# Optimization experiments

Hardware: AMD Instinct MI355X
Metric: run time of the kernel (lower is better)

The kernel has to match this reference:

```python
import jax, jax.numpy as jnp
import numpy as np

H = 256  # LSTM hidden units per layer

def _cell(xt, h, c, W, U, b):
    # Keras LSTMCell: gate order i, f, g(cell), o; sigmoid recurrent activation, tanh activation
    z = xt @ W + h @ U + b  # (B, 4H)
    i, f, g, o = jnp.split(z, 4, axis=-1)
    c_new = jax.nn.sigmoid(f) * c + jax.nn.sigmoid(i) * jnp.tanh(g)
    h_new = jax.nn.sigmoid(o) * jnp.tanh(c_new)
    return h_new, c_new

def _stacked_lstm(x, W1, U1, b1, W2, U2, b2):
    # x: (B, T, F). Returns concat of FINAL CELL STATES of both layers: (B, 2H)
    # (original code takes outputs[i+1][1], i.e. the c state of each LSTMCell)
    B = x.shape[0]
    def step(carry, xt):
        h1, c1, h2, c2 = carry
        h1, c1 = _cell(xt, h1, c1, W1, U1, b1)
        h2, c2 = _cell(h1, h2, c2, W2, U2, b2)
        return (h1, c1, h2, c2), None
    z0 = jnp.zeros((B, H), x.dtype)
    (h1, c1, h2, c2), _ = jax.lax.scan(step, (z0, z0, z0, z0), jnp.swapaxes(x, 0, 1))
    return jnp.concatenate([c1, c2], axis=-1)

def _glorot(key, shape):
    lim = np.sqrt(6.0 / (shape[0] + shape[1]))
    return jax.random.uniform(key, shape, jnp.float32, -lim, lim)

def _lstm_bias():
    # Keras unit_forget_bias=True: forget-gate bias initialized to 1
    return jnp.zeros((4 * H,), jnp.float32).at[H:2 * H].set(1.0)

def setup_inputs():
    key = jax.random.key(0)
    ks = jax.random.split(key, 16)
    B, T, F, ZD = 16384, 20, 80, 32
    inp = {
        "x": jax.random.normal(ks[0], (B, T, F), jnp.float32),
        "eps1": jax.random.normal(ks[1], (B, ZD), jnp.float32),
        "eps2": jax.random.normal(ks[2], (B, ZD), jnp.float32),
        # z2 stacked LSTM (input F)
        "z2_W1": _glorot(ks[3], (F, 4 * H)), "z2_U1": _glorot(ks[4], (H, 4 * H)), "z2_b1": _lstm_bias(),
        "z2_W2": _glorot(ks[5], (H, 4 * H)), "z2_U2": _glorot(ks[6], (H, 4 * H)), "z2_b2": _lstm_bias(),
        # z1 stacked LSTM (input F + z2_dim)
        "z1_W1": _glorot(ks[7], (F + ZD, 4 * H)), "z1_U1": _glorot(ks[8], (H, 4 * H)), "z1_b1": _lstm_bias(),
        "z1_W2": _glorot(ks[9], (H, 4 * H)), "z1_U2": _glorot(ks[10], (H, 4 * H)), "z1_b2": _lstm_bias(),
        # dense heads (input 2H -> ZD), linear (mu_nl=logvar_nl=None)
        "mu2_W": _glorot(ks[11], (2 * H, ZD)), "mu2_b": jnp.zeros((ZD,), jnp.float32),
        "lv2_W": _glorot(ks[12], (2 * H, ZD)), "lv2_b": jnp.zeros((ZD,), jnp.float32),
        "mu1_W": _glorot(ks[13], (2 * H, ZD)), "mu1_b": jnp.zeros((ZD,), jnp.float32),
        "lv1_W": _glorot(ks[14], (2 * H, ZD)), "lv1_b": jnp.zeros((ZD,), jnp.float32),
    }
    return inp

def reference(x, eps1, eps2,
              z2_W1, z2_U1, z2_b1, z2_W2, z2_U2, z2_b2,
              z1_W1, z1_U1, z1_b1, z1_W2, z1_U2, z1_b2,
              mu2_W, mu2_b, lv2_W, lv2_b, mu1_W, mu1_b, lv1_W, lv1_b):
    B, T, _ = x.shape
    # z2 branch
    z2_pre = _stacked_lstm(x, z2_W1, z2_U1, z2_b1, z2_W2, z2_U2, z2_b2)  # (B, 2H)
    z2_mu = z2_pre @ mu2_W + mu2_b
    z2_logvar = z2_pre @ lv2_W + lv2_b
    z2_sample = eps2 * jnp.exp(0.5 * z2_logvar) + z2_mu  # reparameterize
    # z1 branch: tile z2_sample over time, concat with x
    z2_tiled = jnp.broadcast_to(z2_sample[:, None, :], (B, T, z2_sample.shape[-1]))
    x_z2 = jnp.concatenate([x, z2_tiled], axis=-1)  # (B, T, F+ZD)
    z1_pre = _stacked_lstm(x_z2, z1_W1, z1_U1, z1_b1, z1_W2, z1_U2, z1_b2)
    z1_mu = z1_pre @ mu1_W + mu1_b
    z1_logvar = z1_pre @ lv1_W + lv1_b
    z1_sample = eps1 * jnp.exp(0.5 * z1_logvar) + z1_mu
    return (z1_mu, z1_logvar, z1_sample, z2_mu, z2_logvar, z2_sample)
```

## Files before the change

### kernel.cpp

```cpp
#include <hip/hip_runtime.h>
#include <hip/hip_bf16.h>

#define B_SZ 16384
#define T_SZ 20

typedef __attribute__((ext_vector_type(8))) __bf16 bf16x8;
typedef __attribute__((ext_vector_type(4))) float f32x4;

__device__ __forceinline__ float sigm(float x){ return 1.f/(1.f+__expf(-x)); }
__device__ __forceinline__ float tanh_(float x){ return 1.f-2.f/(__expf(2.f*x)+1.f); }

#define OFF_L1Z2 0
#define OFF_L2Z2 360448
#define OFF_L1Z1 884736
#define OFF_L2Z1 1277952
#define OFF_HZ2  1802240
#define OFF_HZ1  1835008
#define WP_TOT   1867776

__global__ void prep_w(const float* __restrict__ W0, const float* __restrict__ U0,
                       const float* __restrict__ W1, const float* __restrict__ U1,
                       const float* __restrict__ W2, const float* __restrict__ U2,
                       const float* __restrict__ W3, const float* __restrict__ U3,
                       const float* __restrict__ muW2, const float* __restrict__ lvW2,
                       const float* __restrict__ muW1, const float* __restrict__ lvW1,
                       __bf16* __restrict__ wp)
{
    int idx = blockIdx.x * 256 + threadIdx.x;
    if (idx >= WP_TOT) return;
    if (idx < OFF_HZ2) {
        const float *W, *U;
        int Fx, Kx, KT, local;
        if (idx < OFF_L2Z2)      { W = W0; U = U0; Fx = 80;  Kx = 96;  KT = 11; local = idx; }
        else if (idx < OFF_L1Z1) { W = W1; U = U1; Fx = 256; Kx = 256; KT = 16; local = idx - OFF_L2Z2; }
        else if (idx < OFF_L2Z1) { W = W2; U = U2; Fx = 112; Kx = 128; KT = 12; local = idx - OFF_L1Z1; }
        else                     { W = W3; U = U3; Fx = 256; Kx = 256; KT = 16; local = idx - OFF_L2Z1; }
        int jj = local & 7, lane = (local >> 3) & 63, nt16 = (local >> 9) & 15, rest = local >> 13;
        int kt = rest % KT, wgn = rest / KT;
        int gate = nt16 & 3, hh = nt16 >> 2;
        int n = gate * 256 + wgn * 64 + hh * 16 + (lane & 15);
        int k = kt * 32 + ((lane >> 4) << 3) + jj;
        float v = (k < Fx) ? W[k * 1024 + n] : (k < Kx ? 0.f : U[(k - Kx) * 1024 + n]);
        wp[idx] = (__bf16)v;
    } else {
        int base = (idx < OFF_HZ1) ? OFF_HZ2 : OFF_HZ1;
        const float* mw = (idx < OFF_HZ1) ? muW2 : muW1;
        const float* lw = (idx < OFF_HZ1) ? lvW2 : lvW1;
        int local = idx - base;
        int jj = local & 7, lane = (local >> 3) & 63, nt = (local >> 9) & 3, kt = local >> 11;
        int k = kt * 32 + ((lane >> 4) << 3) + jj;
        int c16 = lane & 15;
        float v = (nt < 2) ? mw[k * 32 + nt * 16 + c16] : lw[k * 32 + (nt - 2) * 16 + c16];
        wp[idx] = (__bf16)v;
    }
}

__global__ void xconv(const float* __restrict__ x, __bf16* __restrict__ xb)
{
    int idx = blockIdx.x * 256 + threadIdx.x;
    int c8 = idx & 15, row = idx >> 4;
    bf16x8 r;
    if (c8 < 10) {
        const float4* p = reinterpret_cast<const float4*>(x + (size_t)row * 80 + c8 * 8);
        float4 u0 = p[0], u1 = p[1];
        r[0]=(__bf16)u0.x; r[1]=(__bf16)u0.y; r[2]=(__bf16)u0.z; r[3]=(__bf16)u0.w;
        r[4]=(__bf16)u1.x; r[5]=(__bf16)u1.y; r[6]=(__bf16)u1.z; r[7]=(__bf16)u1.w;
    } else {
#pragma unroll
        for (int i = 0; i < 8; ++i) r[i] = (__bf16)0.f;
    }
    *reinterpret_cast<bf16x8*>(xb + (size_t)row * 128 + c8 * 8) = r;
}

__global__ void bcast_z2(const __bf16* __restrict__ z2sb, __bf16* __restrict__ xb)
{
    int idx = blockIdx.x * 256 + threadIdx.x;
    int g = idx & 3, b = idx >> 2;
    bf16x8 v = *reinterpret_cast<const bf16x8*>(z2sb + (size_t)b * 32 + g * 8);
#pragma unroll
    for (int t = 0; t < T_SZ; ++t)
        *reinterpret_cast<bf16x8*>(xb + ((size_t)b * T_SZ + t) * 128 + 80 + g * 8) = v;
}

__device__ __forceinline__ void stage16(const __bf16* g, __bf16* l)
{
    __builtin_amdgcn_global_load_lds(
        (const __attribute__((address_space(1))) unsigned*)g,
        (__attribute__((address_space(3))) unsigned*)l, 16, 0, 0);
}

template <int KT, int KTP, int XKT, int TWOH, int FIRST>
__global__ void __launch_bounds__(512, 2)
step_gemm(const __bf16* __restrict__ xb, int t,
          const __bf16* __restrict__ hA, const __bf16* __restrict__ hB,
          const __bf16* __restrict__ wpm, const float* __restrict__ bias,
          float* __restrict__ cbuf, __bf16* __restrict__ hout)
{
    __shared__ __align__(16) __bf16 As[3][8192];

    const int tid = threadIdx.x;
    const int w = tid >> 6, lane = tid & 63;
    const int r16 = lane & 15, kq = lane >> 4;
    const int wr = w >> 2, wc = w & 3;
    const int mid = blockIdx.x & 63, wgn = blockIdx.x >> 6;
    const int rb = mid * 256;
    const __bf16* wpB = wpm + (size_t)wgn * KTP * 8192;
    const __bf16* pBW = wpB + wc * 2048 + lane * 8;

    const int srow0 = rb + w * 32 + (lane >> 2);
    const int ksub  = (lane & 3) * 8;
    const __bf16* pA0 = hA + (size_t)srow0 * 256 + ksub;
    const __bf16* pA1 = hA + (size_t)(srow0 + 16) * 256 + ksub;
    const __bf16* px0 = (XKT > 0) ? xb + ((size_t)srow0 * T_SZ + t) * 128 + ksub : pA0;
    const __bf16* px1 = (XKT > 0) ? xb + ((size_t)(srow0 + 16) * T_SZ + t) * 128 + ksub : pA1;
    const __bf16* pH0 = TWOH ? hB + (size_t)srow0 * 256 + ksub : pA0;
    const __bf16* pH1 = TWOH ? hB + (size_t)(srow0 + 16) * 256 + ksub : pA1;

    f32x4 acc[4][8];
#pragma unroll
    for (int g = 0; g < 4; ++g)
#pragma unroll
        for (int m = 0; m < 8; ++m) acc[g][m] = f32x4{0.f, 0.f, 0.f, 0.f};

    bf16x8 bR[3][4];

#define ASRC(K, P0, PA, PH_) \
    ((K) < XKT ? (P0) + (K) * 32 \
               : ((!TWOH || ((K) - XKT) < 8) ? (PA) + ((K) - XKT) * 32 \
                                             : (PH_) + ((K) - XKT - 8) * 32))
#define STG_A(K) { stage16(ASRC(K, px0, pA0, pH0), &As[(K) % 3][w * 1024]); \
                   stage16(ASRC(K, px1, pA1, pH1), &As[(K) % 3][w * 1024 + 512]); }
#define LDB(K) { _Pragma("unroll") for (int nt = 0; nt < 4; ++nt) \
                   bR[(K) % 3][nt] = *reinterpret_cast<const bf16x8*>(pBW + (size_t)(K) * 8192 + nt * 512); }
#define CMP(K) { const __bf16* ab_ = &As[(K) % 3][(wr * 128 + r16) * 32 + kq * 8]; \
    bf16x8 a_[8]; \
    _Pragma("unroll") for (int m = 0; m < 8; ++m) \
        a_[m] = *reinterpret_cast<const bf16x8*>(ab_ + m * 512); \
    _Pragma("unroll") for (int m = 0; m < 8; ++m) \
        _Pragma("unroll") for (int g = 0; g < 4; ++g) \
            acc[g][m] = __builtin_amdgcn_mfma_f32_16x16x32_bf16(a_[m], bR[(K) % 3][g], acc[g][m], 0, 0, 0); }
#define PH(K) if constexpr ((K) < KT) { \
    __builtin_amdgcn_sched_barrier(0); \
    if constexpr ((K) + 1 < KT) STG_A((K) + 1); \
    if constexpr ((K) + 2 < KT) LDB((K) + 2); \
    { constexpr int c_ = 2 * (((K) + 1 < KT) ? 1 : 0) + 4 * (((K) + 2 < KT) ? 1 : 0); \
      asm volatile("s_waitcnt vmcnt(%0)" :: "n"(c_) : "memory"); } \
    __builtin_amdgcn_s_barrier(); \
    __builtin_amdgcn_sched_barrier(0); \
    CMP(K); }

    STG_A(0); LDB(0);
    if constexpr (KT > 1) LDB(1);

    PH(0)  PH(1)  PH(2)  PH(3)  PH(4)  PH(5)  PH(6)  PH(7)
    PH(8)  PH(9)  PH(10) PH(11) PH(12) PH(13) PH(14) PH(15)

#undef ASRC
#undef STG_A
#undef LDB
#undef CMP
#undef PH

    const int hcol = wgn * 64 + wc * 16 + r16;
    float bg[4];
#pragma unroll
    for (int g = 0; g < 4; ++g) bg[g] = bias[g * 256 + hcol];

#pragma unroll
    for (int m = 0; m < 8; ++m) {
        f32x4 zi = acc[0][m], zf = acc[1][m], zg = acc[2][m], zo = acc[3][m];
#pragma unroll
        for (int q = 0; q < 4; ++q) {
            int row = rb + wr * 128 + m * 16 + kq * 4 + q;
            size_t off = (size_t)row * 256 + hcol;
            float cn;
            if (FIRST) {
                cn = sigm(zi[q] + bg[0]) * tanh_(zg[q] + bg[2]);
            } else {
                float co = cbuf[off];
                cn = sigm(zf[q] + bg[1]) * co + sigm(zi[q] + bg[0]) * tanh_(zg[q] + bg[2]);
            }
            cbuf[off] = cn;
            hout[off] = (__bf16)(sigm(zo[q] + bg[3]) * tanh_(cn));
        }
    }
}

__global__ void __launch_bounds__(128, 4)
head_mfma(const float* __restrict__ c1, const float* __restrict__ c2,
          const __bf16* __restrict__ hp, const float* __restrict__ mub,
          const float* __restrict__ lvb, const float* __restrict__ eps,
          float* __restrict__ omu, float* __restrict__ olv, float* __restrict__ osm,
          __bf16* __restrict__ osb)
{
    const int tid = threadIdx.x;
    const int w = tid >> 6, lane = tid & 63;
    const int r16 = lane & 15, kq = lane >> 4;
    const int rb = blockIdx.x * 64 + w * 32;

    f32x4 acc[4][2];
#pragma unroll
    for (int nt = 0; nt < 4; ++nt)
#pragma unroll
        for (int m = 0; m < 2; ++m) acc[nt][m] = f32x4{0.f, 0.f, 0.f, 0.f};

#pragma unroll
    for (int kt = 0; kt < 16; ++kt) {
        const float* cs = (kt < 8) ? c1 : c2;
        int k = (kt & 7) * 32 + kq * 8;
        bf16x8 a[2];
#pragma unroll
        for (int m = 0; m < 2; ++m) {
            const float* pr = cs + (size_t)(rb + m * 16 + r16) * 256 + k;
            float4 u0 = reinterpret_cast<const float4*>(pr)[0];
            float4 u1 = reinterpret_cast<const float4*>(pr)[1];
            a[m][0]=(__bf16)u0.x; a[m][1]=(__bf16)u0.y; a[m][2]=(__bf16)u0.z; a[m][3]=(__bf16)u0.w;
            a[m][4]=(__bf16)u1.x; a[m][5]=(__bf16)u1.y; a[m][6]=(__bf16)u1.z; a[m][7]=(__bf16)u1.w;
        }
        const __bf16* hb = hp + kt * 2048 + lane * 8;
#pragma unroll
        for (int nt = 0; nt < 4; ++nt) {
            bf16x8 bv = *reinterpret_cast<const bf16x8*>(hb + nt * 512);
            acc[nt][0] = __builtin_amdgcn_mfma_f32_16x16x32_bf16(a[0], bv, acc[nt][0], 0, 0, 0);
            acc[nt][1] = __builtin_amdgcn_mfma_f32_16x16x32_bf16(a[1], bv, acc[nt][1], 0, 0, 0);
        }
    }

#pragma unroll
    for (int m = 0; m < 2; ++m)
#pragma unroll
        for (int q = 0; q < 4; ++q) {
            int row = rb + m * 16 + kq * 4 + q;
#pragma unroll
            for (int z = 0; z < 2; ++z) {
                int zc = z * 16 + r16;
                float mu = acc[z][m][q] + mub[zc];
                float lv = acc[z + 2][m][q] + lvb[zc];
                int idx = row * 32 + zc;
                omu[idx] = mu;
                olv[idx] = lv;
                float s = fmaf(eps[idx], expf(0.5f * lv), mu);
                osm[idx] = s;
                if (osb) osb[idx] = (__bf16)s;
            }
        }
}

extern "C" void kernel_launch(void* const* d_in, const int* in_sizes, int n_in,
                              void* d_out, int out_size, void* d_ws, size_t ws_size,
                              hipStream_t stream)
{
    const float* x    = (const float*)d_in[0];
    const float* eps1 = (const float*)d_in[1];
    const float* eps2 = (const float*)d_in[2];
    const float* z2W1 = (const float*)d_in[3];
    const float* z2U1 = (const float*)d_in[4];
    const float* z2b1 = (const float*)d_in[5];
    const float* z2W2 = (const float*)d_in[6];
    const float* z2U2 = (const float*)d_in[7];
    const float* z2b2 = (const float*)d_in[8];
    const float* z1W1 = (const float*)d_in[9];
    const float* z1U1 = (const float*)d_in[10];
    const float* z1b1 = (const float*)d_in[11];
    const float* z1W2 = (const float*)d_in[12];
    const float* z1U2 = (const float*)d_in[13];
    const float* z1b2 = (const float*)d_in[14];
    const float* mu2W = (const float*)d_in[15];
    const float* mu2b = (const float*)d_in[16];
    const float* lv2W = (const float*)d_in[17];
    const float* lv2b = (const float*)d_in[18];
    const float* mu1W = (const float*)d_in[19];
    const float* mu1b = (const float*)d_in[20];
    const float* lv1W = (const float*)d_in[21];
    const float* lv1b = (const float*)d_in[22];

    char* ws = (char*)d_ws;
    __bf16* wp   = (__bf16*)ws;
    __bf16* z2sb = (__bf16*)(ws + 4194304);
    __bf16* xb   = (__bf16*)(ws + 5242880);
    __bf16* h1a  = (__bf16*)(ws + 89128960);
    __bf16* h2a  = (__bf16*)(ws + 97517568);
    __bf16* h1b  = (__bf16*)(ws + 105906176);
    __bf16* h2b  = (__bf16*)(ws + 114294784);
    float*  c1   = (float*)(ws + 122683392);
    float*  c2   = (float*)(ws + 139460608);

    __bf16* h1[2] = {h1a, h1b};
    __bf16* h2[2] = {h2a, h2b};

    float* out = (float*)d_out;
    const int BZ = B_SZ * 32;
    float* z1mu = out;           float* z1lv = out + BZ;     float* z1sm = out + 2 * BZ;
    float* z2mu = out + 3 * BZ;  float* z2lv = out + 4 * BZ; float* z2sm = out + 5 * BZ;

    xconv<<<B_SZ * T_SZ * 16 / 256, 256, 0, stream>>>(x, xb);
    prep_w<<<7296, 256, 0, stream>>>(z2W1, z2U1, z2W2, z2U2, z1W1, z1U1, z1W2, z1U2,
                                     mu2W, lv2W, mu1W, lv1W, wp);

    step_gemm<3, 11, 3, 0, 1><<<256, 512, 0, stream>>>(xb, 0, h1a, nullptr,
                                                       wp + OFF_L1Z2, z2b1, c1, h1[0]);
    step_gemm<8, 16, 0, 1, 1><<<256, 512, 0, stream>>>(xb, 0, h1[0], h2a,
                                                       wp + OFF_L2Z2, z2b2, c2, h2[0]);
    for (int t = 1; t < T_SZ; ++t) {
        int cur = t & 1, prv = cur ^ 1;
        step_gemm<11, 11, 3, 0, 0><<<256, 512, 0, stream>>>(xb, t, h1[prv], nullptr,
                                                            wp + OFF_L1Z2, z2b1, c1, h1[cur]);
        step_gemm<16, 16, 0, 1, 0><<<256, 512, 0, stream>>>(xb, t, h1[cur], h2[prv],
                                                            wp + OFF_L2Z2, z2b2, c2, h2[cur]);
    }
    head_mfma<<<256, 128, 0, stream>>>(c1, c2, wp + OFF_HZ2, mu2b, lv2b, eps2,
                                       z2mu, z2lv, z2sm, z2sb);
    bcast_z2<<<B_SZ * 4 / 256, 256, 0, stream>>>(z2sb, xb);

    step_gemm<4, 12, 4, 0, 1><<<256, 512, 0, stream>>>(xb, 0, h1a, nullptr,
                                                       wp + OFF_L1Z1, z1b1, c1, h1[0]);
    step_gemm<8, 16, 0, 1, 1><<<256, 512, 0, stream>>>(xb, 0, h1[0], h2a,
                                                       wp + OFF_L2Z1, z1b2, c2, h2[0]);
    for (int t = 1; t < T_SZ; ++t) {
        int cur = t & 1, prv = cur ^ 1;
        step_gemm<12, 12, 4, 0, 0><<<256, 512, 0, stream>>>(xb, t, h1[prv], nullptr,
                                                            wp + OFF_L1Z1, z1b1, c1, h1[cur]);
        step_gemm<16, 16, 0, 1, 0><<<256, 512, 0, stream>>>(xb, t, h1[cur], h2[prv],
                                                            wp + OFF_L2Z1, z1b2, c2, h2[cur]);
    }
    head_mfma<<<256, 128, 0, stream>>>(c1, c2, wp + OFF_HZ1, mu1b, lv1b, eps1,
                                       z1mu, z1lv, z1sm, nullptr);
}
```

Measured before the change: 2.144 ms.

## Wavefront-pipeline LSTM layers so layer-2 step t runs alongside layer-1 step t+1

Replaces the two serialized per-timestep launches (layer 1, then layer 2) with one fused launch of 512 blocks. Half the blocks compute layer 2 at step t while the other half compute layer 1 at step t+1, with prologue and epilogue launches at the ends of the sequence. This roughly halves the number of launches and doubles the work per launch, so the GPU is better filled and dependent launches wait on each other less. It adds branch divergence at block level and makes the double-buffer indexing of the h buffers more intricate.

```diff
diff --git a/kernel.cpp b/kernel.cpp
--- a/kernel.cpp
+++ b/kernel.cpp
@@ -90,19 +90,17 @@
 }
 
 template <int KT, int KTP, int XKT, int TWOH, int FIRST>
-__global__ void __launch_bounds__(512, 2)
-step_gemm(const __bf16* __restrict__ xb, int t,
+__device__ __forceinline__ void gemm_step(const __bf16* __restrict__ xb, int t,
           const __bf16* __restrict__ hA, const __bf16* __restrict__ hB,
           const __bf16* __restrict__ wpm, const float* __restrict__ bias,
-          float* __restrict__ cbuf, __bf16* __restrict__ hout)
-{
-    __shared__ __align__(16) __bf16 As[3][8192];
-
+          float* __restrict__ cbuf, __bf16* __restrict__ hout,
+          __bf16 (&As)[3][8192], int bidh)
+{
     const int tid = threadIdx.x;
     const int w = tid >> 6, lane = tid & 63;
     const int r16 = lane & 15, kq = lane >> 4;
     const int wr = w >> 2, wc = w & 3;
-    const int mid = blockIdx.x & 63, wgn = blockIdx.x >> 6;
+    const int mid = bidh & 63, wgn = bidh >> 6;
     const int rb = mid * 256;
     const __bf16* wpB = wpm + (size_t)wgn * KTP * 8192;
     const __bf16* pBW = wpB + wc * 2048 + lane * 8;
@@ -186,6 +184,32 @@
     }
 }
 
+template <int XKT, int KT1, int PHASE, int FIRST2>
+__global__ void __launch_bounds__(512, 2)
+fused_step(const __bf16* __restrict__ xb, int t,
+           const __bf16* __restrict__ h1cur, __bf16* __restrict__ h1nxt,
+           const __bf16* __restrict__ h2prv, __bf16* __restrict__ h2cur,
+           const __bf16* __restrict__ wp1, const __bf16* __restrict__ wp2,
+           const float* __restrict__ b1, const float* __restrict__ b2,
+           float* __restrict__ c1, float* __restrict__ c2)
+{
+    __shared__ __align__(16) __bf16 As[3][8192];
+    const int bidh = blockIdx.x & 255;
+
+    if constexpr (PHASE == 0) {
+        gemm_step<XKT, KT1, XKT, 0, 1>(xb, t + 1, h1cur, nullptr, wp1, b1, c1, h1nxt, As, bidh);
+    } else if constexpr (PHASE == 2) {
+        gemm_step<16, 16, 0, 1, 0>(xb, t, h1cur, h2prv, wp2, b2, c2, h2cur, As, bidh);
+    } else {
+        if ((blockIdx.x >> 8) == 0) {
+            constexpr int KT2 = FIRST2 ? 8 : 16;
+            gemm_step<KT2, 16, 0, 1, FIRST2>(xb, t, h1cur, h2prv, wp2, b2, c2, h2cur, As, bidh);
+        } else {
+            gemm_step<KT1, KT1, XKT, 0, 0>(xb, t + 1, h1cur, nullptr, wp1, b1, c1, h1nxt, As, bidh);
+        }
+    }
+}
+
 __global__ void __launch_bounds__(128, 4)
 head_mfma(const float* __restrict__ c1, const float* __restrict__ c2,
           const __bf16* __restrict__ hp, const float* __restrict__ mub,
@@ -279,8 +303,8 @@
     __bf16* z2sb = (__bf16*)(ws + 4194304);
     __bf16* xb   = (__bf16*)(ws + 5242880);
     __bf16* h1a  = (__bf16*)(ws + 89128960);
-    __bf16* h2a  = (__bf16*)(ws + 97517568);
-    __bf16* h1b  = (__bf16*)(ws + 105906176);
+    __bf16* h1b  = (__bf16*)(ws + 97517568);
+    __bf16* h2a  = (__bf16*)(ws + 105906176);
     __bf16* h2b  = (__bf16*)(ws + 114294784);
     float*  c1   = (float*)(ws + 122683392);
     float*  c2   = (float*)(ws + 139460608);
@@ -297,31 +321,37 @@
     prep_w<<<7296, 256, 0, stream>>>(z2W1, z2U1, z2W2, z2U2, z1W1, z1U1, z1W2, z1U2,
                                      mu2W, lv2W, mu1W, lv1W, wp);
 
-    step_gemm<3, 11, 3, 0, 1><<<256, 512, 0, stream>>>(xb, 0, h1a, nullptr,
-                                                       wp + OFF_L1Z2, z2b1, c1, h1[0]);
-    step_gemm<8, 16, 0, 1, 1><<<256, 512, 0, stream>>>(xb, 0, h1[0], h2a,
-                                                       wp + OFF_L2Z2, z2b2, c2, h2[0]);
-    for (int t = 1; t < T_SZ; ++t) {
-        int cur = t & 1, prv = cur ^ 1;
-        step_gemm<11, 11, 3, 0, 0><<<256, 512, 0, stream>>>(xb, t, h1[prv], nullptr,
-                                                            wp + OFF_L1Z2, z2b1, c1, h1[cur]);
-        step_gemm<16, 16, 0, 1, 0><<<256, 512, 0, stream>>>(xb, t, h1[cur], h2[prv],
-                                                            wp + OFF_L2Z2, z2b2, c2, h2[cur]);
+    {
+        const __bf16* wpa = wp + OFF_L1Z2;
+        const __bf16* wpb = wp + OFF_L2Z2;
+        fused_step<3, 11, 0, 0><<<256, 512, 0, stream>>>(xb, -1, h1[0], h1[0], h2[0], h2[0],
+                                                         wpa, wpb, z2b1, z2b2, c1, c2);
+        fused_step<3, 11, 1, 1><<<512, 512, 0, stream>>>(xb, 0, h1[0], h1[1], h2[1], h2[0],
+                                                         wpa, wpb, z2b1, z2b2, c1, c2);
+        for (int t = 1; t < T_SZ - 1; ++t)
+            fused_step<3, 11, 1, 0><<<512, 512, 0, stream>>>(xb, t, h1[t & 1], h1[(t + 1) & 1],
+                                                             h2[(t + 1) & 1], h2[t & 1],
+                                                             wpa, wpb, z2b1, z2b2, c1, c2);
+        fused_step<3, 11, 2, 0><<<256, 512, 0, stream>>>(xb, 19, h1[1], h1[0], h2[0], h2[1],
+                                                         wpa, wpb, z2b1, z2b2, c1, c2);
     }
     head_mfma<<<256, 128, 0, stream>>>(c1, c2, wp + OFF_HZ2, mu2b, lv2b, eps2,
                                        z2mu, z2lv, z2sm, z2sb);
     bcast_z2<<<B_SZ * 4 / 256, 256, 0, stream>>>(z2sb, xb);
 
-    step_gemm<4, 12, 4, 0, 1><<<256, 512, 0, stream>>>(xb, 0, h1a, nullptr,
-                                                       wp + OFF_L1Z1, z1b1, c1, h1[0]);
-    step_gemm<8, 16, 0, 1, 1><<<256, 512, 0, stream>>>(xb, 0, h1[0], h2a,
-                                                       wp + OFF_L2Z1, z1b2, c2, h2[0]);
-    for (int t = 1; t < T_SZ; ++t) {
-        int cur = t & 1, prv = cur ^ 1;
-        step_gemm<12, 12, 4, 0, 0><<<256, 512, 0, stream>>>(xb, t, h1[prv], nullptr,
-                                                            wp + OFF_L1Z1, z1b1, c1, h1[cur]);
-        step_gemm<16, 16, 0, 1, 0><<<256, 512, 0, stream>>>(xb, t, h1[cur], h2[prv],
-                                                            wp + OFF_L2Z1, z1b2, c2, h2[cur]);
+    {
+        const __bf16* wpa = wp + OFF_L1Z1;
+        const __bf16* wpb = wp + OFF_L2Z1;
+        fused_step<4, 12, 0, 0><<<256, 512, 0, stream>>>(xb, -1, h1[0], h1[0], h2[0], h2[0],
+                                                         wpa, wpb, z1b1, z1b2, c1, c2);
+        fused_step<4, 12, 1, 1><<<512, 512, 0, stream>>>(xb, 0, h1[0], h1[1], h2[1], h2[0],
+                                                         wpa, wpb, z1b1, z1b2, c1, c2);
+        for (int t = 1; t < T_SZ - 1; ++t)
+            fused_step<4, 12, 1, 0><<<512, 512, 0, stream>>>(xb, t, h1[t & 1], h1[(t + 1) & 1],
+                                                             h2[(t + 1) & 1], h2[t & 1],
+                                                             wpa, wpb, z1b1, z1b2, c1, c2);
+        fused_step<4, 12, 2, 0><<<256, 512, 0, stream>>>(xb, 19, h1[1], h1[0], h2[0], h2[1],
+                                                         wpa, wpb, z1b1, z1b2, c1, c2);
     }
     head_mfma<<<256, 128, 0, stream>>>(c1, c2, wp + OFF_HZ1, mu1b, lv1b, eps1,
                                        z1mu, z1lv, z1sm, nullptr);
```

After: 2.069 ms, median of 2. 3.5% less time.
